# Performance work log

Hardware: AMD Instinct MI355X
Metric: run time of the kernel (lower is better)

The kernel has to match this reference:

```python
import jax, jax.numpy as jnp
import numpy as np

B, S, HD, HE = 32, 2048, 1024, 1024

def setup_inputs() -> dict:
    key = jax.random.key(0)
    k1, k2, k3, k4, k5, k6 = jax.random.split(key, 6)
    decoder_hidden = jax.random.normal(k1, (B, HD), dtype=jnp.float32)
    encoder_outputs = jax.random.normal(k2, (B, S, HE), dtype=jnp.float32)
    src_mask = jax.random.randint(k3, (B, S), 0, 2) > 0
    # nn.Linear weights stored as [out, in]; apply as x @ W.T
    s_q = 1.0 / np.sqrt(HD)
    s_k = 1.0 / np.sqrt(HE)
    W_query = jax.random.uniform(k4, (HD, HD), jnp.float32, -s_q, s_q)
    W_key = jax.random.uniform(k5, (HD, HE), jnp.float32, -s_k, s_k)
    W_energy = jax.random.uniform(k6, (1, HD), jnp.float32, -s_q, s_q)
    return {
        "decoder_hidden": decoder_hidden,
        "encoder_outputs": encoder_outputs,
        "src_mask": src_mask,
        "W_query": W_query,
        "W_key": W_key,
        "W_energy": W_energy,
    }

def reference(decoder_hidden, encoder_outputs, src_mask, W_query, W_key, W_energy):
    # q: [B, 1, HD], k: [B, S, HD]
    q = (decoder_hidden @ W_query.T)[:, None, :]
    k = jnp.einsum("bse,de->bsd", encoder_outputs, W_key)
    # scores: [B, S] = v^T tanh(q + k)
    scores = jnp.einsum("bsd,d->bs", jnp.tanh(q + k), W_energy[0])
    scores = jnp.where(src_mask, scores, -1e9)
    attn_weights = jax.nn.softmax(scores, axis=-1)
    context = jnp.einsum("bs,bse->be", attn_weights, encoder_outputs)
    return context, attn_weights
```

## Files before the change

kernel.cpp:

```cpp
#include <hip/hip_runtime.h>
#include <hip/hip_bf16.h>


#define NB 32
#define SS 2048
#define HD 1024
#define HE 1024
#define MM (NB * SS)
#define NT 32

typedef float f32x4 __attribute__((ext_vector_type(4)));
typedef short bf16x8 __attribute__((ext_vector_type(8)));
typedef short short4v __attribute__((ext_vector_type(4)));

static __device__ __forceinline__ short f2bf(float f) {
    union { __hip_bfloat16 h; short s; } u;
    u.h = __float2bfloat16(f);
    return u.s;
}

static __device__ __forceinline__ void gload16(const void* g, const void* l) {
    __builtin_amdgcn_global_load_lds(
        (const __attribute__((address_space(1))) void*)(uintptr_t)(g),
        (__attribute__((address_space(3))) void*)(unsigned)(uintptr_t)(l),
        16, 0, 0);
}

__global__ __launch_bounds__(64) void compact_kernel(const int* __restrict__ mask,
                                                     int* __restrict__ idx,
                                                     int* __restrict__ cnt) {
    const int b = blockIdx.x;
    const int lane = threadIdx.x;
    int base = 0;
    for (int s0 = 0; s0 < SS; s0 += 64) {
        const int m = mask[b * SS + s0 + lane];
        const unsigned long long bal = __ballot(m != 0);
        const int rank = __popcll(bal & ((1ull << lane) - 1ull));
        if (m) idx[b * SS + base + rank] = s0 + lane;
        base += (int)__popcll(bal);
    }
    if (lane == 0) cnt[b] = base;
    for (int j = base + lane; j < SS; j += 64) idx[b * SS + j] = 0;
}

__global__ __launch_bounds__(256) void zero_kernel(float* __restrict__ p, int n) {
    const int i = blockIdx.x * 256 + threadIdx.x;
    if (i < n) p[i] = 0.f;
}

__global__ __launch_bounds__(256) void cvt_bf16_kernel(const float* __restrict__ in,
                                                       short* __restrict__ out, int n8) {
    int i = blockIdx.x * 256 + threadIdx.x;
    const int stride = gridDim.x * 256;
    for (; i < n8; i += stride) {
        const f32x4 a = *(const f32x4*)(in + (long)i * 8);
        const f32x4 b = *(const f32x4*)(in + (long)i * 8 + 4);
        bf16x8 o;
        o[0] = f2bf(a[0]); o[1] = f2bf(a[1]); o[2] = f2bf(a[2]); o[3] = f2bf(a[3]);
        o[4] = f2bf(b[0]); o[5] = f2bf(b[1]); o[6] = f2bf(b[2]); o[7] = f2bf(b[3]);
        *(bf16x8*)(out + (long)i * 8) = o;
    }
}

__global__ __launch_bounds__(256) void qproj_kernel(const float* __restrict__ dh,
                                                    const float* __restrict__ Wq,
                                                    float* __restrict__ q) {
    const int wid  = threadIdx.x >> 6;
    const int lane = threadIdx.x & 63;
    const int d    = blockIdx.x * 4 + wid;
    const float* wrow = Wq + (long)d * HD + lane * 16;
    f32x4 w0 = *(const f32x4*)(wrow + 0);
    f32x4 w1 = *(const f32x4*)(wrow + 4);
    f32x4 w2 = *(const f32x4*)(wrow + 8);
    f32x4 w3 = *(const f32x4*)(wrow + 12);
    for (int b = 0; b < NB; ++b) {
        const float* drow = dh + b * HD + lane * 16;
        f32x4 d0 = *(const f32x4*)(drow + 0);
        f32x4 d1 = *(const f32x4*)(drow + 4);
        f32x4 d2 = *(const f32x4*)(drow + 8);
        f32x4 d3 = *(const f32x4*)(drow + 12);
        f32x4 s4 = w0 * d0 + w1 * d1 + w2 * d2 + w3 * d3;
        float dot = s4[0] + s4[1] + s4[2] + s4[3];
        #pragma unroll
        for (int off = 32; off > 0; off >>= 1)
            dot += __shfl_xor(dot, off, 64);
        if (lane == 0) q[b * HD + d] = dot;
    }
}

__global__ __launch_bounds__(512, 2) void score_fused_kernel(const float* __restrict__ enc,
                                                             const short* __restrict__ wkb,
                                                             const float* __restrict__ qv,
                                                             const float* __restrict__ ven,
                                                             const int* __restrict__ idx,
                                                             const int* __restrict__ cnt,
                                                             float* __restrict__ sp) {
    __shared__ __align__(16) short As[2][128 * 32];
    __shared__ __align__(16) short Bs[2][512 * 32];

    const int bid    = blockIdx.x;
    const int xcd    = bid & 7;
    const int slot   = bid >> 3;
    const int mstrip = xcd * 64 + (slot >> 1);
    const int nt     = slot & 1;
    const int bb     = mstrip >> 4;
    const int tile   = mstrip & 15;

    if (tile * 128 >= cnt[bb]) return;

    const int tid  = threadIdx.x;
    const int lane = tid & 63;
    const int wid  = tid >> 6;
    const int wr   = wid >> 2;
    const int wc   = wid & 3;
    const long mbase = (long)bb * SS + tile * 128;
    const int  nbase = nt * 512;

    f32x4 acc[4][8];
    #pragma unroll
    for (int m = 0; m < 4; ++m)
        #pragma unroll
        for (int n = 0; n < 8; ++n)
            acc[m][n] = (f32x4){0.f, 0.f, 0.f, 0.f};

    const int arow = tid >> 3;
    const int r0i = idx[mbase + arow];
    const int r1i = idx[mbase + arow + 64];
    const float* ap0 = enc + ((long)bb * SS + r0i) * HE + (tid & 7) * 4;
    const float* ap1 = enc + ((long)bb * SS + r1i) * HE + (tid & 7) * 4;
    const int as_  = (arow & 3) ^ ((arow >> 2) & 3);
    const int awb  = (((tid & 7) >> 1) ^ as_) * 16 + (tid & 1) * 8;
    const int aw0  = arow * 64 + awb;
    const int aw1  = (arow + 64) * 64 + awb;

    const int bswz = ((tid & 3) ^ ((tid >> 2) & 3) ^ ((tid >> 4) & 3)) * 8;
    const short* bp0 = wkb + (long)(nbase + (tid >> 2)) * HE + bswz;
    const short* bp1 = bp0 + 128 * (long)HE;
    const short* bp2 = bp1 + 128 * (long)HE;
    const short* bp3 = bp2 + 128 * (long)HE;
    const int bd0 = (0 * 512 + wid * 64) * 16;
    const int bd1 = (1 * 512 + wid * 64) * 16;
    const int bd2 = (2 * 512 + wid * 64) * 16;
    const int bd3 = (3 * 512 + wid * 64) * 16;

    const int frow = lane & 15;
    const int kby  = (((lane >> 4) ^ (frow & 3) ^ ((frow >> 2) & 3))) * 16;

    #define BSTAGE(BUF, KT)                                  \
        do {                                                 \
            const int ko_ = (KT) * 32;                       \
            gload16(bp0 + ko_, (char*)Bs[BUF] + bd0);        \
            gload16(bp1 + ko_, (char*)Bs[BUF] + bd1);        \
            gload16(bp2 + ko_, (char*)Bs[BUF] + bd2);        \
            gload16(bp3 + ko_, (char*)Bs[BUF] + bd3);        \
        } while (0)

    #define ACOMMIT(BUF, RA, RB)                                             \
        do {                                                                 \
            short4v v0_, v1_;                                                \
            v0_[0]=f2bf(RA[0]); v0_[1]=f2bf(RA[1]); v0_[2]=f2bf(RA[2]); v0_[3]=f2bf(RA[3]); \
            v1_[0]=f2bf(RB[0]); v1_[1]=f2bf(RB[1]); v1_[2]=f2bf(RB[2]); v1_[3]=f2bf(RB[3]); \
            *(short4v*)((char*)As[BUF] + aw0) = v0_;                         \
            *(short4v*)((char*)As[BUF] + aw1) = v1_;                         \
        } while (0)

    #define COMPUTE(CUR)                                                     \
        do {                                                                 \
            bf16x8 af_[4], bf_[8];                                           \
            _Pragma("unroll")                                                \
            for (int m = 0; m < 4; ++m)                                      \
                af_[m] = *(const bf16x8*)((const char*)As[CUR]               \
                           + (wr * 64 + m * 16 + frow) * 64 + kby);          \
            _Pragma("unroll")                                                \
            for (int n = 0; n < 8; ++n)                                      \
                bf_[n] = *(const bf16x8*)((const char*)Bs[CUR]               \
                           + (wc * 128 + n * 16 + frow) * 64 + kby);         \
            _Pragma("unroll")                                                \
            for (int m = 0; m < 4; ++m)                                      \
                _Pragma("unroll")                                            \
                for (int n = 0; n < 8; ++n)                                  \
                    acc[m][n] = __builtin_amdgcn_mfma_f32_16x16x32_bf16(     \
                        af_[m], bf_[n], acc[m][n], 0, 0, 0);                 \
        } while (0)

    #define PHASE_S(CUR, KT, AH0, AH1, AF0, AF1)                             \
        do {                                                                 \
            BSTAGE((CUR) ^ 1, (KT) + 1);                                     \
            AF0 = *(const f32x4*)(ap0 + ((KT) + 2) * 32);                    \
            AF1 = *(const f32x4*)(ap1 + ((KT) + 2) * 32);                    \
            COMPUTE(CUR);                                                    \
            ACOMMIT((CUR) ^ 1, AH0, AH1);                                    \
            asm volatile("s_waitcnt vmcnt(2) lgkmcnt(0)\n\ts_barrier" ::: "memory"); \
        } while (0)

    f32x4 aE0, aE1, aO0, aO1;
    {
        BSTAGE(0, 0);
        f32x4 p0 = *(const f32x4*)(ap0);
        f32x4 p1 = *(const f32x4*)(ap1);
        ACOMMIT(0, p0, p1);
        aE0 = *(const f32x4*)(ap0 + 32);
        aE1 = *(const f32x4*)(ap1 + 32);
        asm volatile("s_waitcnt lgkmcnt(0)\n\ts_barrier" ::: "memory");
    }

    for (int kt = 0; kt < NT - 4; kt += 2) {
        PHASE_S(0, kt,     aE0, aE1, aO0, aO1);
        PHASE_S(1, kt + 1, aO0, aO1, aE0, aE1);
    }
    PHASE_S(0, NT - 4, aE0, aE1, aO0, aO1);
    PHASE_S(1, NT - 3, aO0, aO1, aE0, aE1);
    {
        BSTAGE(1, NT - 1);
        COMPUTE(0);
        ACOMMIT(1, aE0, aE1);
        asm volatile("s_waitcnt vmcnt(0) lgkmcnt(0)\n\ts_barrier" ::: "memory");
    }
    COMPUTE(1);
    #undef PHASE_S
    #undef COMPUTE
    #undef ACOMMIT
    #undef BSTAGE

    float qq[8], vv[8];
    #pragma unroll
    for (int n = 0; n < 8; ++n) {
        const int c = nbase + wc * 128 + n * 16 + frow;
        qq[n] = qv[bb * HD + c];
        vv[n] = ven[c];
    }
    float p[4][4];
    #pragma unroll
    for (int m = 0; m < 4; ++m) {
        #pragma unroll
        for (int rg = 0; rg < 4; ++rg) {
            float s = 0.f;
            #pragma unroll
            for (int n = 0; n < 8; ++n) {
                const float x = acc[m][n][rg] + qq[n];
                const float e = __expf(2.f * x);
                const float t = 1.f - 2.f * __builtin_amdgcn_rcpf(e + 1.f);
                s += vv[n] * t;
            }
            #pragma unroll
            for (int msk = 1; msk <= 8; msk <<= 1)
                s += __shfl_xor(s, msk, 64);
            p[m][rg] = s;
        }
    }
    if ((lane & 15) == 0) {
        const int g = lane >> 4;
        float* dst = sp + (long)(nt * 4 + wc) * MM;
        #pragma unroll
        for (int m = 0; m < 4; ++m)
            #pragma unroll
            for (int rg = 0; rg < 4; ++rg)
                dst[mbase + wr * 64 + m * 16 + g * 4 + rg] = p[m][rg];
    }
}

__global__ __launch_bounds__(256) void softmax_kernel(const float* __restrict__ sp,
                                                      const int* __restrict__ idx,
                                                      const int* __restrict__ cnt,
                                                      float* __restrict__ attn,
                                                      float* __restrict__ wcomp) {
    const int b = blockIdx.x;
    const int tid = threadIdx.x;
    const int lane = tid & 63;
    const int wid = tid >> 6;
    const int n = cnt[b];
    __shared__ float red[4];
    float sc[8];
    float mx = -3.0e38f;
    #pragma unroll
    for (int i = 0; i < 8; ++i) {
        const int j = tid + i * 256;
        float v = -3.0e38f;
        if (j < n) {
            v = 0.f;
            #pragma unroll
            for (int k = 0; k < 8; ++k)
                v += sp[(long)k * MM + b * SS + j];
        }
        sc[i] = v;
        mx = fmaxf(mx, v);
    }
    #pragma unroll
    for (int off = 32; off > 0; off >>= 1)
        mx = fmaxf(mx, __shfl_xor(mx, off, 64));
    if (lane == 0) red[wid] = mx;
    __syncthreads();
    mx = fmaxf(fmaxf(red[0], red[1]), fmaxf(red[2], red[3]));
    __syncthreads();
    float sum = 0.f;
    #pragma unroll
    for (int i = 0; i < 8; ++i) {
        const float e = (sc[i] > -1.0e38f) ? __expf(sc[i] - mx) : 0.f;
        sc[i] = e;
        sum += e;
    }
    #pragma unroll
    for (int off = 32; off > 0; off >>= 1)
        sum += __shfl_xor(sum, off, 64);
    if (lane == 0) red[wid] = sum;
    __syncthreads();
    sum = red[0] + red[1] + red[2] + red[3];
    const float inv = 1.f / sum;
    #pragma unroll
    for (int i = 0; i < 8; ++i) {
        const int j = tid + i * 256;
        const float w = sc[i] * inv;
        wcomp[b * SS + j] = w;
        if (j < n) attn[b * SS + idx[b * SS + j]] = w;
    }
}

__global__ __launch_bounds__(256) void ctx_partial_kernel(const float* __restrict__ enc,
                                                          const float* __restrict__ wcomp,
                                                          const int* __restrict__ idx,
                                                          const int* __restrict__ cnt,
                                                          float* __restrict__ cp) {
    const int b = blockIdx.x >> 5;
    const int chunk = blockIdx.x & 31;
    const int tid = threadIdx.x;
    float* dst = cp + ((long)(b * 32 + chunk)) * HE + tid * 4;
    if (chunk * 64 >= cnt[b]) {
        *(f32x4*)dst = (f32x4){0.f, 0.f, 0.f, 0.f};
        return;
    }
    f32x4 acc = (f32x4){0.f, 0.f, 0.f, 0.f};
    #pragma unroll 4
    for (int s = 0; s < 64; ++s) {
        const int j = chunk * 64 + s;
        const float w = wcomp[b * SS + j];
        const int row = idx[b * SS + j];
        const f32x4 v = *(const f32x4*)(enc + ((long)b * SS + row) * HE + tid * 4);
        acc += w * v;
    }
    *(f32x4*)dst = acc;
}

__global__ __launch_bounds__(256) void ctx_reduce_kernel(const float* __restrict__ cp,
                                                         float* __restrict__ out) {
    const int o = blockIdx.x * 256 + threadIdx.x;
    const int b = o >> 10;
    const int e = o & 1023;
    float s = 0.f;
    #pragma unroll
    for (int c = 0; c < 32; ++c)
        s += cp[((long)(b * 32 + c)) * HE + e];
    out[o] = s;
}

extern "C" void kernel_launch(void* const* d_in, const int* in_sizes, int n_in,
                              void* d_out, int out_size, void* d_ws, size_t ws_size,
                              hipStream_t stream) {
    const float* dh   = (const float*)d_in[0];
    const float* enc  = (const float*)d_in[1];
    const int*   mask = (const int*)d_in[2];
    const float* Wq   = (const float*)d_in[3];
    const float* Wk   = (const float*)d_in[4];
    const float* Ve   = (const float*)d_in[5];

    float* out  = (float*)d_out;
    float* ctx  = out;
    float* attn = out + NB * HD;

    float* ws    = (float*)d_ws;
    float* wq_   = ws;
    float* sp    = ws + 32768;
    float* cp    = sp + 8 * (long)MM;
    short* wkb   = (short*)(cp + 32 * 32 * HE);
    float* wcomp = (float*)(wkb + (long)HD * HE);
    int*   idx   = (int*)(wcomp + MM);
    int*   cnt   = idx + MM;

    compact_kernel<<<NB, 64, 0, stream>>>(mask, idx, cnt);
    zero_kernel<<<MM / 256, 256, 0, stream>>>(attn, MM);
    qproj_kernel<<<256, 256, 0, stream>>>(dh, Wq, wq_);
    cvt_bf16_kernel<<<512, 256, 0, stream>>>(Wk, wkb, HD * HE / 8);
    score_fused_kernel<<<1024, 512, 0, stream>>>(enc, wkb, wq_, Ve, idx, cnt, sp);
    softmax_kernel<<<NB, 256, 0, stream>>>(sp, idx, cnt, attn, wcomp);
    ctx_partial_kernel<<<1024, 256, 0, stream>>>(enc, wcomp, idx, cnt, cp);
    ctx_reduce_kernel<<<128, 256, 0, stream>>>(cp, ctx);
}
```

Measured before the change: 191.7 us.

## Pre-convert compacted encoder rows to bf16 and simplify score GEMM to 128x128 tiles

Adds a kernel that gathers the masked-in encoder rows and writes them once as contiguous bf16, zero-padding up to a multiple of 128 rows. The score kernel becomes a simpler 128x128-tile MFMA GEMM with 4096 blocks of 256 threads, loading both operands straight into LDS via global_load_lds, single-buffered with two barriers per k-step. The context kernel reads the bf16 compacted copy instead of gathering fp32 rows. The idea is to drop the in-loop fp32-to-bf16 conversion and indirect gathers and to halve the bytes read later, at the cost of an extra pass writing a bf16 copy, lost double buffering, and bf16 rounding in the context sum.

```diff
diff --git a/kernel.cpp b/kernel.cpp
--- a/kernel.cpp
+++ b/kernel.cpp
@@ -17,6 +17,11 @@
     union { __hip_bfloat16 h; short s; } u;
     u.h = __float2bfloat16(f);
     return u.s;
+}
+static __device__ __forceinline__ float bf2f(short s) {
+    union { float f; unsigned u; } u;
+    u.u = ((unsigned)(unsigned short)s) << 16;
+    return u.f;
 }
 
 static __device__ __forceinline__ void gload16(const void* g, const void* l) {
@@ -59,6 +64,36 @@
         o[0] = f2bf(a[0]); o[1] = f2bf(a[1]); o[2] = f2bf(a[2]); o[3] = f2bf(a[3]);
         o[4] = f2bf(b[0]); o[5] = f2bf(b[1]); o[6] = f2bf(b[2]); o[7] = f2bf(b[3]);
         *(bf16x8*)(out + (long)i * 8) = o;
+    }
+}
+
+__global__ __launch_bounds__(256) void cvt_enc_kernel(const float* __restrict__ enc,
+                                                      const int* __restrict__ idx,
+                                                      const int* __restrict__ cnt,
+                                                      short* __restrict__ encb) {
+    const int b  = blockIdx.x >> 7;
+    const int j0 = (blockIdx.x & 127) * 16;
+    const int n  = cnt[b];
+    const int nr = (n + 127) & ~127;
+    if (j0 >= nr) return;
+    const int j  = j0 + (threadIdx.x >> 4);
+    const int c0 = (threadIdx.x & 15) * 8;
+    short* dst = encb + ((long)b * SS + j) * HE + c0;
+    if (j < n) {
+        const float* src = enc + ((long)b * SS + idx[b * SS + j]) * HE + c0;
+        #pragma unroll
+        for (int u = 0; u < 8; ++u) {
+            const f32x4 x = *(const f32x4*)(src + u * 128);
+            const f32x4 y = *(const f32x4*)(src + u * 128 + 4);
+            bf16x8 o;
+            o[0] = f2bf(x[0]); o[1] = f2bf(x[1]); o[2] = f2bf(x[2]); o[3] = f2bf(x[3]);
+            o[4] = f2bf(y[0]); o[5] = f2bf(y[1]); o[6] = f2bf(y[2]); o[7] = f2bf(y[3]);
+            *(bf16x8*)(dst + u * 128) = o;
+        }
+    } else {
+        const bf16x8 z = (bf16x8){0,0,0,0,0,0,0,0};
+        #pragma unroll
+        for (int u = 0; u < 8; ++u) *(bf16x8*)(dst + u * 128) = z;
     }
 }
 
@@ -88,144 +123,75 @@
     }
 }
 
-__global__ __launch_bounds__(512, 2) void score_fused_kernel(const float* __restrict__ enc,
-                                                             const short* __restrict__ wkb,
-                                                             const float* __restrict__ qv,
-                                                             const float* __restrict__ ven,
-                                                             const int* __restrict__ idx,
-                                                             const int* __restrict__ cnt,
-                                                             float* __restrict__ sp) {
-    __shared__ __align__(16) short As[2][128 * 32];
-    __shared__ __align__(16) short Bs[2][512 * 32];
-
-    const int bid    = blockIdx.x;
-    const int xcd    = bid & 7;
-    const int slot   = bid >> 3;
-    const int mstrip = xcd * 64 + (slot >> 1);
-    const int nt     = slot & 1;
-    const int bb     = mstrip >> 4;
-    const int tile   = mstrip & 15;
-
+__global__ __launch_bounds__(256, 3) void score_mfma_kernel(const short* __restrict__ encb,
+                                                            const short* __restrict__ wkb,
+                                                            const float* __restrict__ qv,
+                                                            const float* __restrict__ ven,
+                                                            const int* __restrict__ cnt,
+                                                            float* __restrict__ sp) {
+    __shared__ __align__(16) short As[4096];
+    __shared__ __align__(16) short Bs[4096];
+
+    const int bid   = blockIdx.x;
+    const int xcd   = bid & 7;
+    const int slot  = bid >> 3;
+    const int mtile = xcd * 64 + (slot >> 3);
+    const int nt    = slot & 7;
+
+    const int bb   = mtile >> 4;
+    const int tile = mtile & 15;
     if (tile * 128 >= cnt[bb]) return;
 
     const int tid  = threadIdx.x;
     const int lane = tid & 63;
     const int wid  = tid >> 6;
-    const int wr   = wid >> 2;
-    const int wc   = wid & 3;
+    const int wr   = wid >> 1;
+    const int wc   = wid & 1;
     const long mbase = (long)bb * SS + tile * 128;
-    const int  nbase = nt * 512;
-
-    f32x4 acc[4][8];
+    const int  nbase = nt * 128;
+
+    f32x4 acc[4][4];
     #pragma unroll
     for (int m = 0; m < 4; ++m)
         #pragma unroll
-        for (int n = 0; n < 8; ++n)
+        for (int n = 0; n < 4; ++n)
             acc[m][n] = (f32x4){0.f, 0.f, 0.f, 0.f};
 
-    const int arow = tid >> 3;
-    const int r0i = idx[mbase + arow];
-    const int r1i = idx[mbase + arow + 64];
-    const float* ap0 = enc + ((long)bb * SS + r0i) * HE + (tid & 7) * 4;
-    const float* ap1 = enc + ((long)bb * SS + r1i) * HE + (tid & 7) * 4;
-    const int as_  = (arow & 3) ^ ((arow >> 2) & 3);
-    const int awb  = (((tid & 7) >> 1) ^ as_) * 16 + (tid & 1) * 8;
-    const int aw0  = arow * 64 + awb;
-    const int aw1  = (arow + 64) * 64 + awb;
-
-    const int bswz = ((tid & 3) ^ ((tid >> 2) & 3) ^ ((tid >> 4) & 3)) * 8;
-    const short* bp0 = wkb + (long)(nbase + (tid >> 2)) * HE + bswz;
-    const short* bp1 = bp0 + 128 * (long)HE;
-    const short* bp2 = bp1 + 128 * (long)HE;
-    const short* bp3 = bp2 + 128 * (long)HE;
-    const int bd0 = (0 * 512 + wid * 64) * 16;
-    const int bd1 = (1 * 512 + wid * 64) * 16;
-    const int bd2 = (2 * 512 + wid * 64) * 16;
-    const int bd3 = (3 * 512 + wid * 64) * 16;
+    const short* ag0 = encb + (mbase + (tid >> 2)) * (long)HE + (tid & 3) * 8;
+    const short* ag1 = ag0 + 64 * (long)HE;
+    const short* bg0 = wkb + ((long)(nbase + (tid >> 2))) * HE + (tid & 3) * 8;
+    const short* bg1 = bg0 + 64 * (long)HE;
 
     const int frow = lane & 15;
-    const int kby  = (((lane >> 4) ^ (frow & 3) ^ ((frow >> 2) & 3))) * 16;
-
-    #define BSTAGE(BUF, KT)                                  \
-        do {                                                 \
-            const int ko_ = (KT) * 32;                       \
-            gload16(bp0 + ko_, (char*)Bs[BUF] + bd0);        \
-            gload16(bp1 + ko_, (char*)Bs[BUF] + bd1);        \
-            gload16(bp2 + ko_, (char*)Bs[BUF] + bd2);        \
-            gload16(bp3 + ko_, (char*)Bs[BUF] + bd3);        \
-        } while (0)
-
-    #define ACOMMIT(BUF, RA, RB)                                             \
-        do {                                                                 \
-            short4v v0_, v1_;                                                \
-            v0_[0]=f2bf(RA[0]); v0_[1]=f2bf(RA[1]); v0_[2]=f2bf(RA[2]); v0_[3]=f2bf(RA[3]); \
-            v1_[0]=f2bf(RB[0]); v1_[1]=f2bf(RB[1]); v1_[2]=f2bf(RB[2]); v1_[3]=f2bf(RB[3]); \
-            *(short4v*)((char*)As[BUF] + aw0) = v0_;                         \
-            *(short4v*)((char*)As[BUF] + aw1) = v1_;                         \
-        } while (0)
-
-    #define COMPUTE(CUR)                                                     \
-        do {                                                                 \
-            bf16x8 af_[4], bf_[8];                                           \
-            _Pragma("unroll")                                                \
-            for (int m = 0; m < 4; ++m)                                      \
-                af_[m] = *(const bf16x8*)((const char*)As[CUR]               \
-                           + (wr * 64 + m * 16 + frow) * 64 + kby);          \
-            _Pragma("unroll")                                                \
-            for (int n = 0; n < 8; ++n)                                      \
-                bf_[n] = *(const bf16x8*)((const char*)Bs[CUR]               \
-                           + (wc * 128 + n * 16 + frow) * 64 + kby);         \
-            _Pragma("unroll")                                                \
-            for (int m = 0; m < 4; ++m)                                      \
-                _Pragma("unroll")                                            \
-                for (int n = 0; n < 8; ++n)                                  \
-                    acc[m][n] = __builtin_amdgcn_mfma_f32_16x16x32_bf16(     \
-                        af_[m], bf_[n], acc[m][n], 0, 0, 0);                 \
-        } while (0)
-
-    #define PHASE_S(CUR, KT, AH0, AH1, AF0, AF1)                             \
-        do {                                                                 \
-            BSTAGE((CUR) ^ 1, (KT) + 1);                                     \
-            AF0 = *(const f32x4*)(ap0 + ((KT) + 2) * 32);                    \
-            AF1 = *(const f32x4*)(ap1 + ((KT) + 2) * 32);                    \
-            COMPUTE(CUR);                                                    \
-            ACOMMIT((CUR) ^ 1, AH0, AH1);                                    \
-            asm volatile("s_waitcnt vmcnt(2) lgkmcnt(0)\n\ts_barrier" ::: "memory"); \
-        } while (0)
-
-    f32x4 aE0, aE1, aO0, aO1;
-    {
-        BSTAGE(0, 0);
-        f32x4 p0 = *(const f32x4*)(ap0);
-        f32x4 p1 = *(const f32x4*)(ap1);
-        ACOMMIT(0, p0, p1);
-        aE0 = *(const f32x4*)(ap0 + 32);
-        aE1 = *(const f32x4*)(ap1 + 32);
-        asm volatile("s_waitcnt lgkmcnt(0)\n\ts_barrier" ::: "memory");
-    }
-
-    for (int kt = 0; kt < NT - 4; kt += 2) {
-        PHASE_S(0, kt,     aE0, aE1, aO0, aO1);
-        PHASE_S(1, kt + 1, aO0, aO1, aE0, aE1);
-    }
-    PHASE_S(0, NT - 4, aE0, aE1, aO0, aO1);
-    PHASE_S(1, NT - 3, aO0, aO1, aE0, aE1);
-    {
-        BSTAGE(1, NT - 1);
-        COMPUTE(0);
-        ACOMMIT(1, aE0, aE1);
-        asm volatile("s_waitcnt vmcnt(0) lgkmcnt(0)\n\ts_barrier" ::: "memory");
-    }
-    COMPUTE(1);
-    #undef PHASE_S
-    #undef COMPUTE
-    #undef ACOMMIT
-    #undef BSTAGE
-
-    float qq[8], vv[8];
-    #pragma unroll
-    for (int n = 0; n < 8; ++n) {
-        const int c = nbase + wc * 128 + n * 16 + frow;
+    const int kby  = (lane >> 4) * 16;
+
+    for (int kt = 0; kt < NT; ++kt) {
+        const int ko = kt * 32;
+        gload16(ag0 + ko, (char*)As + wid * 1024);
+        gload16(ag1 + ko, (char*)As + 4096 + wid * 1024);
+        gload16(bg0 + ko, (char*)Bs + wid * 1024);
+        gload16(bg1 + ko, (char*)Bs + 4096 + wid * 1024);
+        __syncthreads();
+
+        bf16x8 af[4], bfr[4];
+        #pragma unroll
+        for (int m = 0; m < 4; ++m)
+            af[m] = *(const bf16x8*)((const char*)As + (wr * 64 + m * 16 + frow) * 64 + kby);
+        #pragma unroll
+        for (int n = 0; n < 4; ++n)
+            bfr[n] = *(const bf16x8*)((const char*)Bs + (wc * 64 + n * 16 + frow) * 64 + kby);
+        #pragma unroll
+        for (int m = 0; m < 4; ++m)
+            #pragma unroll
+            for (int n = 0; n < 4; ++n)
+                acc[m][n] = __builtin_amdgcn_mfma_f32_16x16x32_bf16(af[m], bfr[n], acc[m][n], 0, 0, 0);
+        __syncthreads();
+    }
+
+    float qq[4], vv[4];
+    #pragma unroll
+    for (int n = 0; n < 4; ++n) {
+        const int c = nbase + wc * 64 + n * 16 + frow;
         qq[n] = qv[bb * HD + c];
         vv[n] = ven[c];
     }
@@ -236,7 +202,7 @@
         for (int rg = 0; rg < 4; ++rg) {
             float s = 0.f;
             #pragma unroll
-            for (int n = 0; n < 8; ++n) {
+            for (int n = 0; n < 4; ++n) {
                 const float x = acc[m][n][rg] + qq[n];
                 const float e = __expf(2.f * x);
                 const float t = 1.f - 2.f * __builtin_amdgcn_rcpf(e + 1.f);
@@ -250,7 +216,7 @@
     }
     if ((lane & 15) == 0) {
         const int g = lane >> 4;
-        float* dst = sp + (long)(nt * 4 + wc) * MM;
+        float* dst = sp + (long)(nt * 2 + wc) * MM;
         #pragma unroll
         for (int m = 0; m < 4; ++m)
             #pragma unroll
@@ -279,7 +245,7 @@
         if (j < n) {
             v = 0.f;
             #pragma unroll
-            for (int k = 0; k < 8; ++k)
+            for (int k = 0; k < 16; ++k)
                 v += sp[(long)k * MM + b * SS + j];
         }
         sc[i] = v;
@@ -315,9 +281,8 @@
     }
 }
 
-__global__ __launch_bounds__(256) void ctx_partial_kernel(const float* __restrict__ enc,
+__global__ __launch_bounds__(256) void ctx_partial_kernel(const short* __restrict__ encb,
                                                           const float* __restrict__ wcomp,
-                                                          const int* __restrict__ idx,
                                                           const int* __restrict__ cnt,
                                                           float* __restrict__ cp) {
     const int b = blockIdx.x >> 5;
@@ -328,14 +293,17 @@
         *(f32x4*)dst = (f32x4){0.f, 0.f, 0.f, 0.f};
         return;
     }
+    const short* ep = encb + ((long)b * SS + chunk * 64) * HE + tid * 4;
+    const float* ap = wcomp + b * SS + chunk * 64;
     f32x4 acc = (f32x4){0.f, 0.f, 0.f, 0.f};
     #pragma unroll 4
     for (int s = 0; s < 64; ++s) {
-        const int j = chunk * 64 + s;
-        const float w = wcomp[b * SS + j];
-        const int row = idx[b * SS + j];
-        const f32x4 v = *(const f32x4*)(enc + ((long)b * SS + row) * HE + tid * 4);
-        acc += w * v;
+        const float w = ap[s];
+        const short4v v = *(const short4v*)(ep + (long)s * HE);
+        acc[0] += w * bf2f(v[0]);
+        acc[1] += w * bf2f(v[1]);
+        acc[2] += w * bf2f(v[2]);
+        acc[3] += w * bf2f(v[3]);
     }
     *(f32x4*)dst = acc;
 }
@@ -369,18 +337,20 @@
     float* ws    = (float*)d_ws;
     float* wq_   = ws;
     float* sp    = ws + 32768;
-    float* cp    = sp + 8 * (long)MM;
+    float* cp    = sp + 16 * (long)MM;
     short* wkb   = (short*)(cp + 32 * 32 * HE);
     float* wcomp = (float*)(wkb + (long)HD * HE);
     int*   idx   = (int*)(wcomp + MM);
     int*   cnt   = idx + MM;
+    short* encb  = (short*)(cnt + 64);
 
     compact_kernel<<<NB, 64, 0, stream>>>(mask, idx, cnt);
     zero_kernel<<<MM / 256, 256, 0, stream>>>(attn, MM);
     qproj_kernel<<<256, 256, 0, stream>>>(dh, Wq, wq_);
     cvt_bf16_kernel<<<512, 256, 0, stream>>>(Wk, wkb, HD * HE / 8);
-    score_fused_kernel<<<1024, 512, 0, stream>>>(enc, wkb, wq_, Ve, idx, cnt, sp);
+    cvt_enc_kernel<<<NB * 128, 256, 0, stream>>>(enc, idx, cnt, encb);
+    score_mfma_kernel<<<4096, 256, 0, stream>>>(encb, wkb, wq_, Ve, cnt, sp);
     softmax_kernel<<<NB, 256, 0, stream>>>(sp, idx, cnt, attn, wcomp);
-    ctx_partial_kernel<<<1024, 256, 0, stream>>>(enc, wcomp, idx, cnt, cp);
+    ctx_partial_kernel<<<1024, 256, 0, stream>>>(encb, wcomp, cnt, cp);
     ctx_reduce_kernel<<<128, 256, 0, stream>>>(cp, ctx);
 }
```

Result: faster. 187.6 us (-2.2%).
